# Kernel tuning notes

Hardware: AMD Instinct MI355X
Metric: run time of the kernel (lower is better)

Reference implementation:

```python
import jax, jax.numpy as jnp
import numpy as np

B, N, D = 16, 8192, 256
H = D // 2
N_PARCELS = 64          # number of parcel labels in the stage lookup
K_PER_PARCEL = 32       # allocation m for every parcel (self.values)
TAU = 1.0               # gumbel-softmax temperature


def setup_inputs() -> dict:
    key = jax.random.key(0)
    ks = jax.random.split(key, 6)
    patches = jax.random.normal(ks[0], (B, N, D), dtype=jnp.float32)
    features = jax.random.normal(ks[1], (B, N, D), dtype=jnp.float32)
    W1 = jax.random.normal(ks[2], (D, H), dtype=jnp.float32) * 0.05
    b1 = jnp.zeros((H,), dtype=jnp.float32)
    W2 = jax.random.normal(ks[3], (H,), dtype=jnp.float32) * 0.05  # fc2 weight, out_dim=1 squeezed
    b2 = jnp.zeros((), dtype=jnp.float32)
    # pre-sampled Gumbel(0,1) noise (torch F.gumbel_softmax samples internally)
    gumbel = jax.random.gumbel(ks[4], (B, N), dtype=jnp.float32)
    # flat per-patch parcel label, identical across batch (lookup.reshape(-1)[:N])
    lookup = (jnp.arange(N, dtype=jnp.int32) % N_PARCELS)
    return {"patches": patches, "features": features, "W1": W1, "b1": b1,
            "W2": W2, "b2": b2, "gumbel": gumbel, "lookup": lookup}


def reference(patches, features, W1, b1, W2, b2, gumbel, lookup):
    # tiny MLP: fc1 -> relu -> fc2 -> squeeze(-1)
    hidden = jax.nn.relu(jnp.einsum('bnd,dh->bnh', features, W1) + b1)
    importance_logits = jnp.einsum('bnh,h->bn', hidden, W2) + b2          # [B, N]
    # soft gumbel-softmax scores over the patch axis
    scores = jax.nn.softmax((importance_logits + gumbel) / TAU, axis=-1)  # [B, N]

    labels = jnp.arange(N_PARCELS, dtype=lookup.dtype)

    def per_parcel(label):
        m = lookup == label                                # [N], same for all batches
        masked = jnp.where(m[None, :], scores, -jnp.inf)   # [B, N]
        _, idx = jax.lax.top_k(masked, K_PER_PARCEL)       # [B, K]
        return idx

    idx_pbk = jax.vmap(per_parcel)(labels)                 # [P, B, K]
    all_selected_indices = jnp.transpose(idx_pbk, (1, 0, 2)).reshape(B, N_PARCELS * K_PER_PARCEL)

    # scatter 1.0 at selected positions
    final_mask = jnp.zeros_like(scores).at[jnp.arange(B)[:, None], all_selected_indices].set(1.0)
    # straight-through: value == final_mask, grad flows as -d(logits)
    mask_grad = final_mask + jax.lax.stop_gradient(importance_logits) - importance_logits

    final_patches = patches * mask_grad[..., None]                         # [B, N, D]
    selected_patches = jnp.take_along_axis(final_patches, all_selected_indices[..., None], axis=1)
    return selected_patches, all_selected_indices, importance_logits
```

## Files before the change

kernel.cpp:

```cpp
#include <hip/hip_runtime.h>
#include <hip/hip_bf16.h>

#define NB 16
#define NN 8192
#define ND 256
#define NH 128
#define NPARCEL 64
#define KSEL 32

typedef __attribute__((ext_vector_type(8))) short short8;
typedef __attribute__((ext_vector_type(4))) float floatx4;
typedef __attribute__((ext_vector_type(4))) float f32x4;

__device__ __forceinline__ unsigned short f2b(float x) {
    unsigned u = __builtin_bit_cast(unsigned, x);
    u += 0x7fffu + ((u >> 16) & 1u);
    return (unsigned short)(u >> 16);
}
__device__ __forceinline__ float b2f(unsigned short h) {
    return __builtin_bit_cast(float, (unsigned)h << 16);
}


__global__ __launch_bounds__(256) void k_prep(const float* __restrict__ W1,
                                              unsigned short* __restrict__ W1Th,
                                              unsigned short* __restrict__ W1Tl) {
    int i = blockIdx.x * 256 + threadIdx.x;
    int k = i >> 7;
    int h = i & 127;
    float w = W1[i];
    unsigned short hi = f2b(w);
    float r = w - b2f(hi);
    W1Th[h * ND + k] = hi;
    W1Tl[h * ND + k] = f2b(r);
}

__global__ __launch_bounds__(256) void k_mlp(const float* __restrict__ feat,
                                             const unsigned short* __restrict__ W1Th,
                                             const unsigned short* __restrict__ W1Tl,
                                             const float* __restrict__ b1,
                                             const float* __restrict__ W2,
                                             const float* __restrict__ b2,
                                             float* __restrict__ out_logit) {
    const int wave = threadIdx.x >> 6;
    const int lane = threadIdx.x & 63;
    const int quad = lane >> 4;
    const int m    = lane & 15;
    const int wavebase = blockIdx.x * 128 + wave * 32;

    const unsigned short* bhb = W1Th + m * ND + quad * 8;
    const unsigned short* blb = W1Tl + m * ND + quad * 8;
    const float* ap0 = feat + (size_t)(wavebase + m) * ND + quad * 8;
    const float* ap1 = ap0 + 16 * ND;

    floatx4 acc[2][8];
#pragma unroll
    for (int rg = 0; rg < 2; ++rg)
#pragma unroll
        for (int nt = 0; nt < 8; ++nt) acc[rg][nt] = (floatx4){0.f, 0.f, 0.f, 0.f};

#pragma unroll 1
    for (int k0 = 0; k0 < ND; k0 += 32) {
        f32x4 a00 = *(const f32x4*)(ap0 + k0);
        f32x4 a01 = *(const f32x4*)(ap0 + k0 + 4);
        f32x4 a10 = *(const f32x4*)(ap1 + k0);
        f32x4 a11 = *(const f32x4*)(ap1 + k0 + 4);
        short8 ah0, al0, ah1, al1;
#pragma unroll
        for (int j = 0; j < 8; ++j) {
            float x0 = (j < 4) ? a00[j] : a01[j - 4];
            unsigned short h0 = f2b(x0);
            ah0[j] = (short)h0;
            al0[j] = (short)f2b(x0 - b2f(h0));
            float x1 = (j < 4) ? a10[j] : a11[j - 4];
            unsigned short h1 = f2b(x1);
            ah1[j] = (short)h1;
            al1[j] = (short)f2b(x1 - b2f(h1));
        }
#pragma unroll
        for (int nt = 0; nt < 8; ++nt) {
            short8 bh = *(const short8*)(bhb + nt * 16 * ND + k0);
            short8 bl = *(const short8*)(blb + nt * 16 * ND + k0);
            acc[0][nt] = __builtin_amdgcn_mfma_f32_16x16x32_bf16(ah0, bh, acc[0][nt], 0, 0, 0);
            acc[0][nt] = __builtin_amdgcn_mfma_f32_16x16x32_bf16(ah0, bl, acc[0][nt], 0, 0, 0);
            acc[0][nt] = __builtin_amdgcn_mfma_f32_16x16x32_bf16(al0, bh, acc[0][nt], 0, 0, 0);
            acc[1][nt] = __builtin_amdgcn_mfma_f32_16x16x32_bf16(ah1, bh, acc[1][nt], 0, 0, 0);
            acc[1][nt] = __builtin_amdgcn_mfma_f32_16x16x32_bf16(ah1, bl, acc[1][nt], 0, 0, 0);
            acc[1][nt] = __builtin_amdgcn_mfma_f32_16x16x32_bf16(al1, bh, acc[1][nt], 0, 0, 0);
        }
    }

    const float b2v = b2[0];
#pragma unroll
    for (int rg = 0; rg < 2; ++rg) {
        float s[4] = {0.f, 0.f, 0.f, 0.f};
#pragma unroll
        for (int nt = 0; nt < 8; ++nt) {
            float b1f = b1[nt * 16 + m];
            float w2f = W2[nt * 16 + m];
#pragma unroll
            for (int r = 0; r < 4; ++r) {
                float h = acc[rg][nt][r] + b1f;
                s[r] += (h > 0.f ? h : 0.f) * w2f;
            }
        }
#pragma unroll
        for (int off = 1; off < 16; off <<= 1) {
#pragma unroll
            for (int r = 0; r < 4; ++r) s[r] += __shfl_xor(s[r], off, 64);
        }
        if (m == 0) {
            int rowbase = wavebase + rg * 16 + quad * 4;
#pragma unroll
            for (int r = 0; r < 4; ++r) {
                int row = rowbase + r;
                out_logit[row] = s[r] + b2v;
            }
        }
    }
}

__global__ __launch_bounds__(256) void k_topk_gather(const float* __restrict__ logit,
                                                     const float* __restrict__ gum,
                                                     const float* __restrict__ patches,
                                                     float* __restrict__ out_sel,
                                                     float* __restrict__ out_idx) {
    const int b = blockIdx.x >> 6;
    const int p = blockIdx.x & 63;
    const int t = threadIdx.x;
    const int g = t >> 6;
    const int l = t & 63;

    const float* lb = logit + b * NN;
    const float* gb = gum + b * NN;
    int i0 = p + 64 * l;
    int i1 = i0 + 4096;
    float v0 = lb[i0] + gb[i0];
    float v1 = lb[i1] + gb[i1];
    const int obase = b * (NPARCEL * KSEL) + p * KSEL;

    int idxs[8];
#pragma unroll
    for (int r = 0; r < KSEL; ++r) {
        float bv; int bi;
        if (v0 > v1 || (v0 == v1 && i0 < i1)) { bv = v0; bi = i0; }
        else                                  { bv = v1; bi = i1; }
#pragma unroll
        for (int off = 1; off < 64; off <<= 1) {
            float ov = __shfl_xor(bv, off, 64);
            int   oi = __shfl_xor(bi, off, 64);
            if (ov > bv || (ov == bv && oi < bi)) { bv = ov; bi = oi; }
        }
        if      (bi == i0) { v0 = -__builtin_inff(); i0 = 0x7fffffff; }
        else if (bi == i1) { v1 = -__builtin_inff(); i1 = 0x7fffffff; }
        int safe = bi & (NN - 1);
        if (t == r) out_idx[obase + r] = (float)safe;
        if ((r & 3) == g) idxs[r >> 2] = safe;
    }

#pragma unroll
    for (int rr = 0; rr < 8; ++rr) {
        const int r = rr * 4 + g;
        f32x4 v = *((const f32x4*)(patches + ((size_t)b * NN + idxs[rr]) * ND) + l);
        *((f32x4*)(out_sel + (size_t)(obase + r) * ND) + l) = v;
    }
}

extern "C" void kernel_launch(void* const* d_in, const int* in_sizes, int n_in,
                              void* d_out, int out_size, void* d_ws, size_t ws_size,
                              hipStream_t stream) {
    const float* patches = (const float*)d_in[0];
    const float* feat    = (const float*)d_in[1];
    const float* W1      = (const float*)d_in[2];
    const float* b1      = (const float*)d_in[3];
    const float* W2      = (const float*)d_in[4];
    const float* b2      = (const float*)d_in[5];
    const float* gum     = (const float*)d_in[6];

    float* out       = (float*)d_out;
    float* out_sel   = out;
    float* out_idx   = out + 8388608;
    float* out_logit = out + 8388608 + 32768;

    unsigned short* W1Th = (unsigned short*)(out_sel);
    unsigned short* W1Tl = (unsigned short*)(out_sel + 16384);

    k_prep<<<128, 256, 0, stream>>>(W1, W1Th, W1Tl);
    k_mlp<<<(NB * NN) / 128, 256, 0, stream>>>(feat, W1Th, W1Tl, b1, W2, b2, out_logit);
    k_topk_gather<<<NB * NPARCEL, 256, 0, stream>>>(out_logit, gum, patches, out_sel, out_idx);
}
```

Baseline: 341.1 us.

## Stage W1 hi/lo bf16 halves in swizzled LDS and prefetch feature loads

The MLP kernel now copies the transposed W1 hi and lo bf16 planes into 64 KB of XOR-swizzled shared memory in two K-phases. It then reads the B operands from LDS instead of issuing global loads per wave per tile. The feature loads for the next K step are software-prefetched into registers while the current step's MFMAs run. This is meant to cut redundant global/L2 traffic for weights and hide load latency, at the cost of a large LDS footprint that limits occupancy, plus extra barriers.

```diff
diff --git a/kernel.cpp b/kernel.cpp
--- a/kernel.cpp
+++ b/kernel.cpp
@@ -23,35 +23,35 @@
 
 
 __global__ __launch_bounds__(256) void k_prep(const float* __restrict__ W1,
-                                              unsigned short* __restrict__ W1Th,
-                                              unsigned short* __restrict__ W1Tl) {
+                                              unsigned short* __restrict__ W1T) {
     int i = blockIdx.x * 256 + threadIdx.x;
     int k = i >> 7;
     int h = i & 127;
     float w = W1[i];
     unsigned short hi = f2b(w);
     float r = w - b2f(hi);
-    W1Th[h * ND + k] = hi;
-    W1Tl[h * ND + k] = f2b(r);
-}
-
-__global__ __launch_bounds__(256) void k_mlp(const float* __restrict__ feat,
-                                             const unsigned short* __restrict__ W1Th,
-                                             const unsigned short* __restrict__ W1Tl,
-                                             const float* __restrict__ b1,
-                                             const float* __restrict__ W2,
-                                             const float* __restrict__ b2,
-                                             float* __restrict__ out_logit) {
+    W1T[h * ND + k] = hi;
+    W1T[32768 + h * ND + k] = f2b(r);
+}
+
+__global__ __launch_bounds__(256, 2) void k_mlp(const float* __restrict__ feat,
+                                                const unsigned short* __restrict__ W1T,
+                                                const float* __restrict__ b1,
+                                                const float* __restrict__ W2,
+                                                const float* __restrict__ b2,
+                                                float* __restrict__ out_logit) {
+    __shared__ f32x4 lds4[4096];
+    unsigned char* lds = (unsigned char*)lds4;
+
     const int wave = threadIdx.x >> 6;
     const int lane = threadIdx.x & 63;
     const int quad = lane >> 4;
     const int m    = lane & 15;
     const int wavebase = blockIdx.x * 128 + wave * 32;
 
-    const unsigned short* bhb = W1Th + m * ND + quad * 8;
-    const unsigned short* blb = W1Tl + m * ND + quad * 8;
     const float* ap0 = feat + (size_t)(wavebase + m) * ND + quad * 8;
     const float* ap1 = ap0 + 16 * ND;
+    const int swz = (m & 7) << 4;
 
     floatx4 acc[2][8];
 #pragma unroll
@@ -59,34 +59,60 @@
 #pragma unroll
         for (int nt = 0; nt < 8; ++nt) acc[rg][nt] = (floatx4){0.f, 0.f, 0.f, 0.f};
 
+    f32x4 a00 = *(const f32x4*)(ap0);
+    f32x4 a01 = *(const f32x4*)(ap0 + 4);
+    f32x4 a10 = *(const f32x4*)(ap1);
+    f32x4 a11 = *(const f32x4*)(ap1 + 4);
+
 #pragma unroll 1
-    for (int k0 = 0; k0 < ND; k0 += 32) {
-        f32x4 a00 = *(const f32x4*)(ap0 + k0);
-        f32x4 a01 = *(const f32x4*)(ap0 + k0 + 4);
-        f32x4 a10 = *(const f32x4*)(ap1 + k0);
-        f32x4 a11 = *(const f32x4*)(ap1 + k0 + 4);
-        short8 ah0, al0, ah1, al1;
-#pragma unroll
-        for (int j = 0; j < 8; ++j) {
-            float x0 = (j < 4) ? a00[j] : a01[j - 4];
-            unsigned short h0 = f2b(x0);
-            ah0[j] = (short)h0;
-            al0[j] = (short)f2b(x0 - b2f(h0));
-            float x1 = (j < 4) ? a10[j] : a11[j - 4];
-            unsigned short h1 = f2b(x1);
-            ah1[j] = (short)h1;
-            al1[j] = (short)f2b(x1 - b2f(h1));
-        }
-#pragma unroll
-        for (int nt = 0; nt < 8; ++nt) {
-            short8 bh = *(const short8*)(bhb + nt * 16 * ND + k0);
-            short8 bl = *(const short8*)(blb + nt * 16 * ND + k0);
-            acc[0][nt] = __builtin_amdgcn_mfma_f32_16x16x32_bf16(ah0, bh, acc[0][nt], 0, 0, 0);
-            acc[0][nt] = __builtin_amdgcn_mfma_f32_16x16x32_bf16(ah0, bl, acc[0][nt], 0, 0, 0);
-            acc[0][nt] = __builtin_amdgcn_mfma_f32_16x16x32_bf16(al0, bh, acc[0][nt], 0, 0, 0);
-            acc[1][nt] = __builtin_amdgcn_mfma_f32_16x16x32_bf16(ah1, bh, acc[1][nt], 0, 0, 0);
-            acc[1][nt] = __builtin_amdgcn_mfma_f32_16x16x32_bf16(ah1, bl, acc[1][nt], 0, 0, 0);
-            acc[1][nt] = __builtin_amdgcn_mfma_f32_16x16x32_bf16(al1, bh, acc[1][nt], 0, 0, 0);
+    for (int ph = 0; ph < 2; ++ph) {
+        if (ph) __syncthreads();
+#pragma unroll
+        for (int i = 0; i < 16; ++i) {
+            int c  = threadIdx.x + i * 256;
+            int pl = c >> 11;
+            int h  = (c >> 4) & 127;
+            f32x4 v = *(const f32x4*)((const unsigned char*)W1T +
+                                      pl * 65536 + h * 512 + ph * 256 + (c & 15) * 16);
+            *(f32x4*)(lds + ((c * 16) ^ ((h & 7) << 4))) = v;
+        }
+        __syncthreads();
+
+#pragma unroll 1
+        for (int kk = 0; kk < 128; kk += 32) {
+            const int k0 = ph * 128 + kk;
+            const int kn = (k0 + 32) & 255;
+            f32x4 n00 = *(const f32x4*)(ap0 + kn);
+            f32x4 n01 = *(const f32x4*)(ap0 + kn + 4);
+            f32x4 n10 = *(const f32x4*)(ap1 + kn);
+            f32x4 n11 = *(const f32x4*)(ap1 + kn + 4);
+
+            short8 ah0, al0, ah1, al1;
+#pragma unroll
+            for (int j = 0; j < 8; ++j) {
+                float x0 = (j < 4) ? a00[j] : a01[j - 4];
+                unsigned short h0 = f2b(x0);
+                ah0[j] = (short)h0;
+                al0[j] = (short)f2b(x0 - b2f(h0));
+                float x1 = (j < 4) ? a10[j] : a11[j - 4];
+                unsigned short h1 = f2b(x1);
+                ah1[j] = (short)h1;
+                al1[j] = (short)f2b(x1 - b2f(h1));
+            }
+
+            const int rb = (m * 256 + quad * 16 + kk * 2) ^ swz;
+#pragma unroll
+            for (int nt = 0; nt < 8; ++nt) {
+                short8 bh = *(const short8*)(lds + (rb + nt * 4096));
+                short8 bl = *(const short8*)(lds + (rb + nt * 4096 + 32768));
+                acc[0][nt] = __builtin_amdgcn_mfma_f32_16x16x32_bf16(ah0, bh, acc[0][nt], 0, 0, 0);
+                acc[0][nt] = __builtin_amdgcn_mfma_f32_16x16x32_bf16(ah0, bl, acc[0][nt], 0, 0, 0);
+                acc[0][nt] = __builtin_amdgcn_mfma_f32_16x16x32_bf16(al0, bh, acc[0][nt], 0, 0, 0);
+                acc[1][nt] = __builtin_amdgcn_mfma_f32_16x16x32_bf16(ah1, bh, acc[1][nt], 0, 0, 0);
+                acc[1][nt] = __builtin_amdgcn_mfma_f32_16x16x32_bf16(ah1, bl, acc[1][nt], 0, 0, 0);
+                acc[1][nt] = __builtin_amdgcn_mfma_f32_16x16x32_bf16(al1, bh, acc[1][nt], 0, 0, 0);
+            }
+            a00 = n00; a01 = n01; a10 = n10; a11 = n11;
         }
     }
 
@@ -182,10 +208,9 @@
     float* out_idx   = out + 8388608;
     float* out_logit = out + 8388608 + 32768;
 
-    unsigned short* W1Th = (unsigned short*)(out_sel);
-    unsigned short* W1Tl = (unsigned short*)(out_sel + 16384);
-
-    k_prep<<<128, 256, 0, stream>>>(W1, W1Th, W1Tl);
-    k_mlp<<<(NB * NN) / 128, 256, 0, stream>>>(feat, W1Th, W1Tl, b1, W2, b2, out_logit);
+    unsigned short* W1T = (unsigned short*)(out_sel);
+
+    k_prep<<<128, 256, 0, stream>>>(W1, W1T);
+    k_mlp<<<(NB * NN) / 128, 256, 0, stream>>>(feat, W1T, b1, W2, b2, out_logit);
     k_topk_gather<<<NB * NPARCEL, 256, 0, stream>>>(out_logit, gum, patches, out_sel, out_idx);
 }
```

New measurement: 308.4 us. -9.6%, faster.

## Stage swizzled split-bf16 W1 tiles in LDS for MLP MFMA loop

Applied to the files above, without the earlier changes.

The prep kernel now writes the hi/lo bf16 halves of transposed W1 into four 32KB K-chunks with an XOR swizzle. The MLP kernel copies each chunk cooperatively into shared memory and reads the B operands from LDS instead of global memory. The goal is to cut repeated global/L2 reads of W1 by every wave and avoid LDS bank conflicts. This costs extra barriers and 32KB of LDS per block, which limits occupancy; launch bounds now request 4 blocks per CU.

```diff
diff --git a/kernel.cpp b/kernel.cpp
--- a/kernel.cpp
+++ b/kernel.cpp
@@ -23,35 +23,42 @@
 
 
 __global__ __launch_bounds__(256) void k_prep(const float* __restrict__ W1,
-                                              unsigned short* __restrict__ W1Th,
-                                              unsigned short* __restrict__ W1Tl) {
+                                              unsigned short* __restrict__ W1S) {
     int i = blockIdx.x * 256 + threadIdx.x;
     int k = i >> 7;
     int h = i & 127;
     float w = W1[i];
     unsigned short hi = f2b(w);
-    float r = w - b2f(hi);
-    W1Th[h * ND + k] = hi;
-    W1Tl[h * ND + k] = f2b(r);
-}
-
-__global__ __launch_bounds__(256) void k_mlp(const float* __restrict__ feat,
-                                             const unsigned short* __restrict__ W1Th,
-                                             const unsigned short* __restrict__ W1Tl,
-                                             const float* __restrict__ b1,
-                                             const float* __restrict__ W2,
-                                             const float* __restrict__ b2,
-                                             float* __restrict__ out_logit) {
-    const int wave = threadIdx.x >> 6;
-    const int lane = threadIdx.x & 63;
+    unsigned short lo = f2b(w - b2f(hi));
+    int p   = k >> 6;
+    int kk6 = k & 63;
+    int swz = (h & 7) << 4;
+    unsigned char* base = (unsigned char*)W1S + p * 32768;
+    int linh = h * 128 + kk6 * 2;
+    int linl = 16384 + linh;
+    *(unsigned short*)(base + (linh ^ swz)) = hi;
+    *(unsigned short*)(base + (linl ^ swz)) = lo;
+}
+
+__global__ __launch_bounds__(256, 4) void k_mlp(const float* __restrict__ feat,
+                                                const unsigned short* __restrict__ W1S,
+                                                const float* __restrict__ b1,
+                                                const float* __restrict__ W2,
+                                                const float* __restrict__ b2,
+                                                float* __restrict__ out_logit) {
+    __shared__ f32x4 lds4[2048];
+    unsigned char* lds = (unsigned char*)lds4;
+
+    const int tid  = threadIdx.x;
+    const int wave = tid >> 6;
+    const int lane = tid & 63;
     const int quad = lane >> 4;
     const int m    = lane & 15;
     const int wavebase = blockIdx.x * 128 + wave * 32;
 
-    const unsigned short* bhb = W1Th + m * ND + quad * 8;
-    const unsigned short* blb = W1Tl + m * ND + quad * 8;
     const float* ap0 = feat + (size_t)(wavebase + m) * ND + quad * 8;
     const float* ap1 = ap0 + 16 * ND;
+    const int swz = (m & 7) << 4;
 
     floatx4 acc[2][8];
 #pragma unroll
@@ -60,33 +67,46 @@
         for (int nt = 0; nt < 8; ++nt) acc[rg][nt] = (floatx4){0.f, 0.f, 0.f, 0.f};
 
 #pragma unroll 1
-    for (int k0 = 0; k0 < ND; k0 += 32) {
-        f32x4 a00 = *(const f32x4*)(ap0 + k0);
-        f32x4 a01 = *(const f32x4*)(ap0 + k0 + 4);
-        f32x4 a10 = *(const f32x4*)(ap1 + k0);
-        f32x4 a11 = *(const f32x4*)(ap1 + k0 + 4);
-        short8 ah0, al0, ah1, al1;
-#pragma unroll
-        for (int j = 0; j < 8; ++j) {
-            float x0 = (j < 4) ? a00[j] : a01[j - 4];
-            unsigned short h0 = f2b(x0);
-            ah0[j] = (short)h0;
-            al0[j] = (short)f2b(x0 - b2f(h0));
-            float x1 = (j < 4) ? a10[j] : a11[j - 4];
-            unsigned short h1 = f2b(x1);
-            ah1[j] = (short)h1;
-            al1[j] = (short)f2b(x1 - b2f(h1));
-        }
-#pragma unroll
-        for (int nt = 0; nt < 8; ++nt) {
-            short8 bh = *(const short8*)(bhb + nt * 16 * ND + k0);
-            short8 bl = *(const short8*)(blb + nt * 16 * ND + k0);
-            acc[0][nt] = __builtin_amdgcn_mfma_f32_16x16x32_bf16(ah0, bh, acc[0][nt], 0, 0, 0);
-            acc[0][nt] = __builtin_amdgcn_mfma_f32_16x16x32_bf16(ah0, bl, acc[0][nt], 0, 0, 0);
-            acc[0][nt] = __builtin_amdgcn_mfma_f32_16x16x32_bf16(al0, bh, acc[0][nt], 0, 0, 0);
-            acc[1][nt] = __builtin_amdgcn_mfma_f32_16x16x32_bf16(ah1, bh, acc[1][nt], 0, 0, 0);
-            acc[1][nt] = __builtin_amdgcn_mfma_f32_16x16x32_bf16(ah1, bl, acc[1][nt], 0, 0, 0);
-            acc[1][nt] = __builtin_amdgcn_mfma_f32_16x16x32_bf16(al1, bh, acc[1][nt], 0, 0, 0);
+    for (int p = 0; p < 4; ++p) {
+        if (p) __syncthreads();
+        const f32x4* src = (const f32x4*)((const unsigned char*)W1S + p * 32768);
+#pragma unroll
+        for (int i = 0; i < 8; ++i) lds4[tid + i * 256] = src[tid + i * 256];
+        __syncthreads();
+
+#pragma unroll 1
+        for (int kx = 0; kx < 2; ++kx) {
+            const int k0 = p * 64 + kx * 32;
+            f32x4 a00 = *(const f32x4*)(ap0 + k0);
+            f32x4 a01 = *(const f32x4*)(ap0 + k0 + 4);
+            f32x4 a10 = *(const f32x4*)(ap1 + k0);
+            f32x4 a11 = *(const f32x4*)(ap1 + k0 + 4);
+
+            short8 ah0, al0, ah1, al1;
+#pragma unroll
+            for (int j = 0; j < 8; ++j) {
+                float x0 = (j < 4) ? a00[j] : a01[j - 4];
+                unsigned short h0 = f2b(x0);
+                ah0[j] = (short)h0;
+                al0[j] = (short)f2b(x0 - b2f(h0));
+                float x1 = (j < 4) ? a10[j] : a11[j - 4];
+                unsigned short h1 = f2b(x1);
+                ah1[j] = (short)h1;
+                al1[j] = (short)f2b(x1 - b2f(h1));
+            }
+
+            const int rb = (m * 128 + quad * 16 + kx * 64) ^ swz;
+#pragma unroll
+            for (int nt = 0; nt < 8; ++nt) {
+                short8 bh = *(const short8*)(lds + (rb + nt * 2048));
+                short8 bl = *(const short8*)(lds + (rb + nt * 2048 + 16384));
+                acc[0][nt] = __builtin_amdgcn_mfma_f32_16x16x32_bf16(ah0, bh, acc[0][nt], 0, 0, 0);
+                acc[0][nt] = __builtin_amdgcn_mfma_f32_16x16x32_bf16(ah0, bl, acc[0][nt], 0, 0, 0);
+                acc[0][nt] = __builtin_amdgcn_mfma_f32_16x16x32_bf16(al0, bh, acc[0][nt], 0, 0, 0);
+                acc[1][nt] = __builtin_amdgcn_mfma_f32_16x16x32_bf16(ah1, bh, acc[1][nt], 0, 0, 0);
+                acc[1][nt] = __builtin_amdgcn_mfma_f32_16x16x32_bf16(ah1, bl, acc[1][nt], 0, 0, 0);
+                acc[1][nt] = __builtin_amdgcn_mfma_f32_16x16x32_bf16(al1, bh, acc[1][nt], 0, 0, 0);
+            }
         }
     }
 
@@ -182,10 +202,9 @@
     float* out_idx   = out + 8388608;
     float* out_logit = out + 8388608 + 32768;
 
-    unsigned short* W1Th = (unsigned short*)(out_sel);
-    unsigned short* W1Tl = (unsigned short*)(out_sel + 16384);
-
-    k_prep<<<128, 256, 0, stream>>>(W1, W1Th, W1Tl);
-    k_mlp<<<(NB * NN) / 128, 256, 0, stream>>>(feat, W1Th, W1Tl, b1, W2, b2, out_logit);
+    unsigned short* W1S = (unsigned short*)(out_sel);
+
+    k_prep<<<128, 256, 0, stream>>>(W1, W1S);
+    k_mlp<<<(NB * NN) / 128, 256, 0, stream>>>(feat, W1S, b1, W2, b2, out_logit);
     k_topk_gather<<<NB * NPARCEL, 256, 0, stream>>>(out_logit, gum, patches, out_sel, out_idx);
 }
```

New measurement: 305.8 us. 10.4% less time.
